# Optimization experiments

Hardware: AMD Instinct MI355X
Metric: run time of the kernel (lower is better)

The kernel has to match this reference:

```python
import jax, jax.numpy as jnp
import numpy as np

EMBED_DIM = 1024

def setup_inputs() -> dict:
    key = jax.random.key(0)
    ks = jax.random.split(key, 7)
    D = EMBED_DIM
    x = jax.random.normal(ks[0], (4, 2048, D), dtype=jnp.float32)
    s = 1.0 / np.sqrt(D)
    Wq = jax.random.normal(ks[1], (D, D), dtype=jnp.float32) * s
    bq = jnp.zeros((D,), dtype=jnp.float32)
    Wk = jax.random.normal(ks[2], (D, D), dtype=jnp.float32) * s
    bk = jnp.zeros((D,), dtype=jnp.float32)
    Wv = jax.random.normal(ks[3], (D, D), dtype=jnp.float32) * s
    bv = jnp.zeros((D,), dtype=jnp.float32)
    return {"x": x, "Wq": Wq, "bq": bq, "Wk": Wk, "bk": bk, "Wv": Wv, "bv": bv}

def reference(x, Wq, bq, Wk, bk, Wv, bv):
    # x: [B,S,D]; torch Linear: x @ W.T + b -> here W is stored as [D_in, D_out]
    Q = jnp.einsum('bsd,de->bse', x, Wq) + bq
    K = jnp.einsum('bsd,de->bse', x, Wk) + bk
    V = jnp.einsum('bsd,de->bse', x, Wv) + bv
    scale = 1.0 / jnp.sqrt(jnp.asarray(x.shape[-1], dtype=x.dtype))
    scores = jnp.einsum('bqd,bkd->bqk', Q, K) * scale  # [B,S,S]
    probs = jax.nn.softmax(scores, axis=-1)
    # dropout is identity in eval mode
    return jnp.einsum('bqk,bkd->bqd', probs, V)
```

## Files before the change

### kernel.cpp

```cpp
#include <hip/hip_runtime.h>
#include <hip/hip_bf16.h>
#include <hip/hip_fp16.h>
#include <stdint.h>
#include <stddef.h>
#include <string.h>

#define D_EMB 1024
#define SEQ   2048
#define BATCH 4

typedef short bf16x8  __attribute__((ext_vector_type(8)));
typedef short short8  __attribute__((ext_vector_type(8)));
typedef float f32x4   __attribute__((ext_vector_type(4)));

#define AS1 __attribute__((address_space(1)))
#define AS3 __attribute__((address_space(3)))

static __device__ __forceinline__ void async_copy16(const void* g, void* l) {
  __builtin_amdgcn_global_load_lds((const AS1 void*)g, (AS3 void*)l, 16, 0, 0);
}

static __device__ __forceinline__ void gemm128(
    const __hip_bfloat16* __restrict__ A, int lda,
    const __hip_bfloat16* __restrict__ Bt, int ldb,
    int K, f32x4 (&acc)[4][4])
{
  __shared__ __hip_bfloat16 ldsA[2][128 * 64];
  __shared__ __hip_bfloat16 ldsB[2][128 * 64];

  const int t    = threadIdx.x;
  const int wave = t >> 6;
  const int lane = t & 63;
  const int quad = lane >> 4;
  const int lr   = lane & 15;
  const int wr   = wave >> 1;
  const int wc   = wave & 1;

  const int r0 = t >> 3;
  const int c0 = (((t & 7) ^ (r0 & 7)) * 8);

  const __hip_bfloat16* gA = A  + (size_t)r0 * lda + c0;
  const __hip_bfloat16* gB = Bt + (size_t)r0 * ldb + c0;

  const int niter = K >> 6;

  {
    char* lA = (char*)ldsA[0] + wave * 1024;
    char* lB = (char*)ldsB[0] + wave * 1024;
#pragma unroll
    for (int ch = 0; ch < 4; ch++) {
      async_copy16(gA + (size_t)(32 * ch) * lda, lA + 4096 * ch);
      async_copy16(gB + (size_t)(32 * ch) * ldb, lB + 4096 * ch);
    }
  }

  int buf = 0;
  for (int it = 0; it < niter; ++it) {
    __syncthreads();

    if (it + 1 < niter) {
      const int k0 = (it + 1) << 6;
      char* lA = (char*)ldsA[buf ^ 1] + wave * 1024;
      char* lB = (char*)ldsB[buf ^ 1] + wave * 1024;
#pragma unroll
      for (int ch = 0; ch < 4; ch++) {
        async_copy16(gA + k0 + (size_t)(32 * ch) * lda, lA + 4096 * ch);
        async_copy16(gB + k0 + (size_t)(32 * ch) * ldb, lB + 4096 * ch);
      }
    }

    const __hip_bfloat16* bA = ldsA[buf];
    const __hip_bfloat16* bB = ldsB[buf];
#pragma unroll
    for (int kk = 0; kk < 64; kk += 32) {
      bf16x8 aF[4], bF[4];
      const int lc = (kk >> 3) + quad;
      const int pc = (lc ^ (lr & 7)) * 8;
#pragma unroll
      for (int i = 0; i < 4; i++)
        aF[i] = *(const bf16x8*)&bA[(wr * 64 + i * 16 + lr) * 64 + pc];
#pragma unroll
      for (int j = 0; j < 4; j++)
        bF[j] = *(const bf16x8*)&bB[(wc * 64 + j * 16 + lr) * 64 + pc];

#pragma unroll
      for (int i = 0; i < 4; i++)
#pragma unroll
        for (int j = 0; j < 4; j++)
          acc[i][j] = __builtin_amdgcn_mfma_f32_16x16x32_bf16(aF[i], bF[j], acc[i][j], 0, 0, 0);
    }
    buf ^= 1;
  }
}

#define ZERO_ACC(acc)                         \
  {                                           \
    f32x4 _z = {0.f, 0.f, 0.f, 0.f};          \
    _Pragma("unroll")                         \
    for (int _i = 0; _i < 4; _i++)            \
      _Pragma("unroll")                       \
      for (int _j = 0; _j < 4; _j++)          \
        acc[_i][_j] = _z;                     \
  }

__global__ __launch_bounds__(256) void prep_kernel(
    const float* __restrict__ x,
    const float* __restrict__ Wq,
    const float* __restrict__ Wk,
    const float* __restrict__ Wv,
    __hip_bfloat16* __restrict__ xb,
    __hip_bfloat16* __restrict__ Wt3)
{
  const int tx = threadIdx.x, ty = threadIdx.y;
  if (blockIdx.z == 3) {
    const int tid = ty * 32 + tx;
    const size_t base = ((size_t)blockIdx.y * 32 + blockIdx.x) * 8192;
#pragma unroll
    for (int p = 0; p < 8; p++) {
      const size_t i = base + p * 1024 + tid * 4;
      const float4 v = *(const float4*)(x + i);
      __hip_bfloat16 o[4] = {__float2bfloat16(v.x), __float2bfloat16(v.y),
                             __float2bfloat16(v.z), __float2bfloat16(v.w)};
      *(uint64_t*)(xb + i) = *(uint64_t*)o;
    }
    return;
  }
  const float* src = (blockIdx.z == 0) ? Wq : (blockIdx.z == 1) ? Wk : Wv;
  __hip_bfloat16* dst = Wt3 + (size_t)blockIdx.z * D_EMB * D_EMB;
  __shared__ __hip_bfloat16 tile[32][33];
  const int x0 = blockIdx.x * 32;
  const int y0 = blockIdx.y * 32;
#pragma unroll
  for (int i = 0; i < 32; i += 8)
    tile[ty + i][tx] = __float2bfloat16(src[(size_t)(y0 + ty + i) * D_EMB + (x0 + tx)]);
  __syncthreads();
#pragma unroll
  for (int i = 0; i < 32; i += 8)
    dst[(size_t)(x0 + ty + i) * D_EMB + (y0 + tx)] = tile[tx][ty + i];
}

__global__ __launch_bounds__(256) void qkv_kernel(
    const __hip_bfloat16* __restrict__ xb,
    const __hip_bfloat16* __restrict__ Wt3,
    const float* __restrict__ bq,
    const float* __restrict__ bk,
    const float* __restrict__ bv,
    __hip_bfloat16* __restrict__ Q,
    __hip_bfloat16* __restrict__ Kb,
    __hip_bfloat16* __restrict__ Vt)
{
  const int mat = blockIdx.z;
  const int m0  = blockIdx.x * 128;
  const int n0  = blockIdx.y * 128;

  f32x4 acc[4][4];
  ZERO_ACC(acc);

  gemm128(xb + (size_t)m0 * D_EMB, D_EMB,
          Wt3 + (size_t)mat * D_EMB * D_EMB + (size_t)n0 * D_EMB, D_EMB,
          D_EMB, acc);

  const float* bias = (mat == 0) ? bq : (mat == 1) ? bk : bv;

  const int t = threadIdx.x;
  const int wave = t >> 6, lane = t & 63;
  const int quad = lane >> 4, lr = lane & 15;
  const int wr = wave >> 1, wc = wave & 1;

#pragma unroll
  for (int i = 0; i < 4; i++) {
#pragma unroll
    for (int j = 0; j < 4; j++) {
      const int n = n0 + wc * 64 + j * 16 + lr;
      const float bb = bias[n];
      const int mbase = m0 + wr * 64 + i * 16 + quad * 4;
      if (mat == 2) {
        const int b = mbase >> 11, s = mbase & 2047;
        __hip_bfloat16 pk[4];
#pragma unroll
        for (int r = 0; r < 4; r++) pk[r] = __float2bfloat16(acc[i][j][r] + bb);
        *(uint64_t*)&Vt[(size_t)b * D_EMB * SEQ + (size_t)n * SEQ + s] = *(uint64_t*)pk;
      } else {
        __hip_bfloat16* dst = (mat == 0) ? Q : Kb;
#pragma unroll
        for (int r = 0; r < 4; r++)
          dst[(size_t)(mbase + r) * D_EMB + n] = __float2bfloat16(acc[i][j][r] + bb);
      }
    }
  }
}

__global__ __launch_bounds__(256) void scores_kernel(
    const __hip_bfloat16* __restrict__ Q,
    const __hip_bfloat16* __restrict__ Kb,
    __half* __restrict__ Sc)
{
  const int b  = blockIdx.z;
  const int m0 = blockIdx.y * 128;
  const int n0 = blockIdx.x * 128;

  f32x4 acc[4][4];
  ZERO_ACC(acc);

  gemm128(Q  + (size_t)b * SEQ * D_EMB + (size_t)m0 * D_EMB, D_EMB,
          Kb + (size_t)b * SEQ * D_EMB + (size_t)n0 * D_EMB, D_EMB,
          D_EMB, acc);

  __half* out = Sc + (size_t)b * SEQ * SEQ;
  const float scale = 0.03125f;

  const int t = threadIdx.x;
  const int wave = t >> 6, lane = t & 63;
  const int quad = lane >> 4, lr = lane & 15;
  const int wr = wave >> 1, wc = wave & 1;

#pragma unroll
  for (int i = 0; i < 4; i++)
#pragma unroll
    for (int j = 0; j < 4; j++) {
      const int n = n0 + wc * 64 + j * 16 + lr;
#pragma unroll
      for (int r = 0; r < 4; r++) {
        const int m = m0 + wr * 64 + i * 16 + quad * 4 + r;
        out[(size_t)m * SEQ + n] = __float2half(acc[i][j][r] * scale);
      }
    }
}

__global__ __launch_bounds__(256) void softmax_kernel(
    const __half* __restrict__ Sc, __hip_bfloat16* __restrict__ P)
{
  const int row = blockIdx.x;
  const __half* src = Sc + (size_t)row * SEQ;
  const int t = threadIdx.x;
  const int wave = t >> 6, lane = t & 63;

  const short8 raw = *(const short8*)(src + t * 8);
  float v[8];
#pragma unroll
  for (int i = 0; i < 8; i++) {
    const short si = raw[i];
    __half h;
    memcpy(&h, &si, sizeof(h));
    v[i] = __half2float(h);
  }

  float m = v[0];
#pragma unroll
  for (int i = 1; i < 8; i++) m = fmaxf(m, v[i]);
#pragma unroll
  for (int o = 32; o > 0; o >>= 1) m = fmaxf(m, __shfl_xor(m, o));

  __shared__ float redm[4];
  __shared__ float reds[4];
  if (lane == 0) redm[wave] = m;
  __syncthreads();
  m = fmaxf(fmaxf(redm[0], redm[1]), fmaxf(redm[2], redm[3]));

  float e[8], s = 0.f;
#pragma unroll
  for (int i = 0; i < 8; i++) { e[i] = __expf(v[i] - m); s += e[i]; }
#pragma unroll
  for (int o = 32; o > 0; o >>= 1) s += __shfl_xor(s, o);
  if (lane == 0) reds[wave] = s;
  __syncthreads();
  s = reds[0] + reds[1] + reds[2] + reds[3];

  const float inv = 1.f / s;
  short8 outp;
#pragma unroll
  for (int i = 0; i < 8; i++) {
    const __hip_bfloat16 b = __float2bfloat16(e[i] * inv);
    short sb;
    memcpy(&sb, &b, sizeof(sb));
    outp[i] = sb;
  }
  *(short8*)(P + (size_t)row * SEQ + t * 8) = outp;
}

__global__ __launch_bounds__(256) void pv_kernel(
    const __hip_bfloat16* __restrict__ P,
    const __hip_bfloat16* __restrict__ Vt,
    float* __restrict__ out)
{
  const int b  = blockIdx.z;
  const int m0 = blockIdx.y * 128;
  const int n0 = blockIdx.x * 128;

  f32x4 acc[4][4];
  ZERO_ACC(acc);

  gemm128(P  + (size_t)b * SEQ * SEQ   + (size_t)m0 * SEQ, SEQ,
          Vt + (size_t)b * D_EMB * SEQ + (size_t)n0 * SEQ, SEQ,
          SEQ, acc);

  float* o = out + (size_t)b * SEQ * D_EMB;

  const int t = threadIdx.x;
  const int wave = t >> 6, lane = t & 63;
  const int quad = lane >> 4, lr = lane & 15;
  const int wr = wave >> 1, wc = wave & 1;

#pragma unroll
  for (int i = 0; i < 4; i++)
#pragma unroll
    for (int j = 0; j < 4; j++) {
      const int n = n0 + wc * 64 + j * 16 + lr;
#pragma unroll
      for (int r = 0; r < 4; r++) {
        const int m = m0 + wr * 64 + i * 16 + quad * 4 + r;
        o[(size_t)m * D_EMB + n] = acc[i][j][r];
      }
    }
}

extern "C" void kernel_launch(void* const* d_in, const int* in_sizes, int n_in,
                              void* d_out, int out_size, void* d_ws, size_t ws_size,
                              hipStream_t stream) {
  const float* x  = (const float*)d_in[0];
  const float* Wq = (const float*)d_in[1];
  const float* bq = (const float*)d_in[2];
  const float* Wk = (const float*)d_in[3];
  const float* bk = (const float*)d_in[4];
  const float* Wv = (const float*)d_in[5];
  const float* bv = (const float*)d_in[6];
  float* out = (float*)d_out;

  char* ws = (char*)d_ws;
  __hip_bfloat16* xb  = (__hip_bfloat16*)(ws);
  __hip_bfloat16* Wt3 = (__hip_bfloat16*)(ws + 16777216);
  __hip_bfloat16* Q   = (__hip_bfloat16*)(ws + 23068672);
  __hip_bfloat16* Kb  = (__hip_bfloat16*)(ws + 39845888);
  __hip_bfloat16* Vt  = (__hip_bfloat16*)(ws + 56623104);
  __half*         Sc  = (__half*)        (ws + 73400320);
  __hip_bfloat16* P   = (__hip_bfloat16*)(ws + 140509184);

  prep_kernel  <<<dim3(32, 32, 4), dim3(32, 8), 0, stream>>>(x, Wq, Wk, Wv, xb, Wt3);
  qkv_kernel   <<<dim3(64, 8, 3),  256,        0, stream>>>(xb, Wt3, bq, bk, bv, Q, Kb, Vt);
  scores_kernel<<<dim3(16, 16, 4), 256,        0, stream>>>(Q, Kb, Sc);
  softmax_kernel<<<dim3(8192),     256,        0, stream>>>(Sc, P);
  pv_kernel    <<<dim3(8, 16, 4),  256,        0, stream>>>(P, Vt, out);
}
```

Baseline: 267.6 us.

## Load B operand fragments directly from global memory and swap grid block order

The shared GEMM routine no longer stages the B tile in LDS. Each lane now reads its bf16x8 B fragments straight from global memory, row by row, halving LDS usage and removing the B async copies. The scores and PV kernels also swap which grid dimension indexes M and N, which changes block scheduling order and L2 reuse of operands. Direct global B loads are not double-buffered and are duplicated across the two waves sharing a column, so load latency sits on the MFMA critical path and redundant global traffic increases.

```diff
diff --git a/kernel.cpp b/kernel.cpp
--- a/kernel.cpp
+++ b/kernel.cpp
@@ -26,7 +26,6 @@
     int K, f32x4 (&acc)[4][4])
 {
   __shared__ __hip_bfloat16 ldsA[2][128 * 64];
-  __shared__ __hip_bfloat16 ldsB[2][128 * 64];
 
   const int t    = threadIdx.x;
   const int wave = t >> 6;
@@ -39,38 +38,35 @@
   const int r0 = t >> 3;
   const int c0 = (((t & 7) ^ (r0 & 7)) * 8);
 
-  const __hip_bfloat16* gA = A  + (size_t)r0 * lda + c0;
-  const __hip_bfloat16* gB = Bt + (size_t)r0 * ldb + c0;
+  const __hip_bfloat16* gA = A + (size_t)r0 * lda + c0;
+
+  const __hip_bfloat16* bRow0 = Bt + (size_t)(wc * 64 +  0 + lr) * ldb + quad * 8;
+  const __hip_bfloat16* bRow1 = Bt + (size_t)(wc * 64 + 16 + lr) * ldb + quad * 8;
+  const __hip_bfloat16* bRow2 = Bt + (size_t)(wc * 64 + 32 + lr) * ldb + quad * 8;
+  const __hip_bfloat16* bRow3 = Bt + (size_t)(wc * 64 + 48 + lr) * ldb + quad * 8;
 
   const int niter = K >> 6;
 
   {
     char* lA = (char*)ldsA[0] + wave * 1024;
-    char* lB = (char*)ldsB[0] + wave * 1024;
-#pragma unroll
-    for (int ch = 0; ch < 4; ch++) {
+#pragma unroll
+    for (int ch = 0; ch < 4; ch++)
       async_copy16(gA + (size_t)(32 * ch) * lda, lA + 4096 * ch);
-      async_copy16(gB + (size_t)(32 * ch) * ldb, lB + 4096 * ch);
-    }
   }
 
   int buf = 0;
   for (int it = 0; it < niter; ++it) {
+    const int k0 = it << 6;
     __syncthreads();
 
     if (it + 1 < niter) {
-      const int k0 = (it + 1) << 6;
       char* lA = (char*)ldsA[buf ^ 1] + wave * 1024;
-      char* lB = (char*)ldsB[buf ^ 1] + wave * 1024;
-#pragma unroll
-      for (int ch = 0; ch < 4; ch++) {
-        async_copy16(gA + k0 + (size_t)(32 * ch) * lda, lA + 4096 * ch);
-        async_copy16(gB + k0 + (size_t)(32 * ch) * ldb, lB + 4096 * ch);
-      }
+#pragma unroll
+      for (int ch = 0; ch < 4; ch++)
+        async_copy16(gA + (k0 + 64) + (size_t)(32 * ch) * lda, lA + 4096 * ch);
     }
 
     const __hip_bfloat16* bA = ldsA[buf];
-    const __hip_bfloat16* bB = ldsB[buf];
 #pragma unroll
     for (int kk = 0; kk < 64; kk += 32) {
       bf16x8 aF[4], bF[4];
@@ -79,9 +75,10 @@
 #pragma unroll
       for (int i = 0; i < 4; i++)
         aF[i] = *(const bf16x8*)&bA[(wr * 64 + i * 16 + lr) * 64 + pc];
-#pragma unroll
-      for (int j = 0; j < 4; j++)
-        bF[j] = *(const bf16x8*)&bB[(wc * 64 + j * 16 + lr) * 64 + pc];
+      bF[0] = *(const bf16x8*)&bRow0[k0 + kk];
+      bF[1] = *(const bf16x8*)&bRow1[k0 + kk];
+      bF[2] = *(const bf16x8*)&bRow2[k0 + kk];
+      bF[3] = *(const bf16x8*)&bRow3[k0 + kk];
 
 #pragma unroll
       for (int i = 0; i < 4; i++)
@@ -196,8 +193,8 @@
     __half* __restrict__ Sc)
 {
   const int b  = blockIdx.z;
-  const int m0 = blockIdx.y * 128;
-  const int n0 = blockIdx.x * 128;
+  const int m0 = blockIdx.x * 128;
+  const int n0 = blockIdx.y * 128;
 
   f32x4 acc[4][4];
   ZERO_ACC(acc);
@@ -284,8 +281,8 @@
     float* __restrict__ out)
 {
   const int b  = blockIdx.z;
-  const int m0 = blockIdx.y * 128;
-  const int n0 = blockIdx.x * 128;
+  const int m0 = blockIdx.x * 128;
+  const int n0 = blockIdx.y * 128;
 
   f32x4 acc[4][4];
   ZERO_ACC(acc);
@@ -339,5 +336,5 @@
   qkv_kernel   <<<dim3(64, 8, 3),  256,        0, stream>>>(xb, Wt3, bq, bk, bv, Q, Kb, Vt);
   scores_kernel<<<dim3(16, 16, 4), 256,        0, stream>>>(Q, Kb, Sc);
   softmax_kernel<<<dim3(8192),     256,        0, stream>>>(Sc, P);
-  pv_kernel    <<<dim3(8, 16, 4),  256,        0, stream>>>(P, Vt, out);
-}
+  pv_kernel    <<<dim3(16, 8, 4),  256,        0, stream>>>(P, Vt, out);
+}
```

New measurement: 370.1 us. +38.3%, slower.
